# Kernel optimization log

Hardware: AMD Instinct MI355X
Metric: run time of the kernel (lower is better)

## Reference

```python
import jax, jax.numpy as jnp
import numpy as np

N_BISECT_ITERS = 50  # entmax_bisect default


def entmax15_bisect(x):
    """1.5-entmax over the last axis via bisection (alpha=1.5 => p(z)=relu(z)^2)."""
    X = x * 0.5  # multiply by (alpha - 1)
    d = X.shape[-1]
    max_val = jnp.max(X, axis=-1, keepdims=True)
    tau_lo = max_val - 1.0                      # gp(1, alpha) = 1
    tau_hi = max_val - (1.0 / d) ** 0.5         # gp(1/d, alpha)
    f_lo = jnp.sum(jnp.square(jnp.clip(X - tau_lo, 0.0)), -1, keepdims=True) - 1.0

    def body(i, carry):
        tau_lo, dm = carry
        dm = dm * 0.5
        tau_m = tau_lo + dm
        f_m = jnp.sum(jnp.square(jnp.clip(X - tau_m, 0.0)), -1, keepdims=True) - 1.0
        tau_lo = jnp.where(f_m * f_lo >= 0, tau_m, tau_lo)
        return (tau_lo, dm)

    tau_lo, dm = jax.lax.fori_loop(0, N_BISECT_ITERS, body, (tau_lo, tau_hi - tau_lo))
    p = jnp.square(jnp.clip(X - (tau_lo + 0.5 * dm), 0.0))
    return p / jnp.sum(p, axis=-1, keepdims=True)


def entmax_adj(x):
    p = entmax15_bisect(x)
    # straight-through argmax -> one-hot
    k = jnp.argmax(p, axis=-1)
    y_hard = jax.nn.one_hot(k, p.shape[-1], dtype=p.dtype)
    return y_hard - jax.lax.stop_gradient(p) + p


def setup_inputs() -> dict:
    key = jax.random.key(0)
    ks = jax.random.split(key, 7)
    N, D_IN, D_EMB = 524288, 200, 100
    x = jax.random.normal(ks[0], (N, D_IN), dtype=jnp.float32)
    # torch Linear init: U(-1/sqrt(fan_in), 1/sqrt(fan_in))
    def lin(k, out_f, in_f):
        kw, kb = jax.random.split(k)
        bound = 1.0 / np.sqrt(in_f)
        w = jax.random.uniform(kw, (out_f, in_f), jnp.float32, -bound, bound)
        b = jax.random.uniform(kb, (out_f,), jnp.float32, -bound, bound)
        return w, b
    w_out, b_out = lin(ks[1], D_EMB, D_IN)      # fc_out: 200 -> 100
    w_cat, b_cat = lin(ks[2], 2, D_EMB)         # fc_cat: 100 -> 2
    w2, b2 = lin(ks[3], 1, 2)                   # fc2: 2 -> 1
    return {"x": x, "w_out": w_out, "b_out": b_out,
            "w_cat": w_cat, "b_cat": b_cat, "w2": w2, "b2": b2}


def reference(x, w_out, b_out, w_cat, b_cat, w2, b2):
    h = jax.nn.relu(x @ w_out.T + b_out)        # [N, 100]
    logits = h @ w_cat.T + b_cat                # [N, 2]
    adj = entmax_adj(logits)                    # [N, 2] one-hot (straight-through)
    return adj @ w2.T + b2                      # [N, 1]
```

## Files before the change

kernel.cpp:

```cpp
#include <hip/hip_runtime.h>

#define DIN 200
#define DH  100
#define NKT 7
#define MARGIN 2e-3f
#define TR   32
#define NT   8
#define RPB  (NT * TR)

typedef _Float16 half8 __attribute__((ext_vector_type(8)));
typedef _Float16 half4 __attribute__((ext_vector_type(4)));
typedef float f32x4 __attribute__((ext_vector_type(4)));

__device__ inline half8 cvt8(float4 u, float4 v) {
  half8 h;
  h[0] = (_Float16)u.x; h[1] = (_Float16)u.y;
  h[2] = (_Float16)u.z; h[3] = (_Float16)u.w;
  h[4] = (_Float16)v.x; h[5] = (_Float16)v.y;
  h[6] = (_Float16)v.z; h[7] = (_Float16)v.w;
  return h;
}
__device__ inline half4 cvt4(float4 u) {
  half4 h;
  h[0] = (_Float16)u.x; h[1] = (_Float16)u.y;
  h[2] = (_Float16)u.z; h[3] = (_Float16)u.w;
  return h;
}

template <bool HAVE_WS>
__global__ __launch_bounds__(256, 4)
void entmax_sign_mfma(const float* __restrict__ x,
                      const float* __restrict__ w_out,
                      const float* __restrict__ b_out,
                      const float* __restrict__ w_cat,
                      const float* __restrict__ b_cat,
                      const float* __restrict__ w2,
                      const float* __restrict__ b2,
                      float* __restrict__ out,
                      unsigned* __restrict__ cnt,
                      int* __restrict__ list) {
  __shared__ _Float16 axf[14 * 512];
  __shared__ float parts[2][4][TR];

  const int tid  = threadIdx.x;
  const int lane = tid & 63;
  const int wid  = tid >> 6;
  const int arow = lane & 15;
  const int qid  = lane >> 4;

  const float db = b_cat[0] - b_cat[1];
  const float c0 = w2[0] + b2[0];
  const float c1 = w2[1] + b2[0];

  for (int t2 = tid; t2 < 768; t2 += 256) {
    const int fi = t2 / 384, r2 = t2 - fi * 384;
    axf[(fi * 7 + 6) * 512 + 128 + r2] = (_Float16)0.f;
  }

  half8 wf0[NKT], wf1[NKT];
  float bjv0, djv0, bjv1, djv1;
  {
    const int j0 = (2 * wid) * 16 + arow;
    const int j1 = (2 * wid + 1) * 16 + arow;
    bjv0 = (j0 < DH) ? b_out[j0] : 0.f;
    djv0 = (j0 < DH) ? (w_cat[j0] - w_cat[DH + j0]) : 0.f;
    bjv1 = (j1 < DH) ? b_out[j1] : 0.f;
    djv1 = (j1 < DH) ? (w_cat[j1] - w_cat[DH + j1]) : 0.f;
#pragma unroll
    for (int kt = 0; kt < NKT; ++kt) {
      const int k = kt * 32 + qid * 8;
      half8 h0 = {}, h1 = {};
      if (k < DIN) {
        if (j0 < DH) {
          float4 a = *(const float4*)(w_out + j0 * DIN + k);
          float4 b = *(const float4*)(w_out + j0 * DIN + k + 4);
          h0 = cvt8(a, b);
        }
        if (j1 < DH) {
          float4 a = *(const float4*)(w_out + j1 * DIN + k);
          float4 b = *(const float4*)(w_out + j1 * DIN + k + 4);
          h1 = cvt8(a, b);
        }
      }
      wf0[kt] = h0; wf1[kt] = h1;
    }
  }

  const int blockBase = blockIdx.x * RPB;
  const float4* xf4 = (const float4*)x;

  const int row_l = tid & 31;
  const int cseg  = tid >> 5;
  const int wbase = (row_l >> 4) * 7 * 512 + ((row_l & 15) + (cseg >> 1) * 16) * 8
                  + (cseg & 1) * 4;

  float4 u0, u1, u2, u3, u4, u5, u6;
#define LOADT(T)                                                            \
  {                                                                         \
    const float4* xt = xf4 + (size_t)(blockBase + (T) * TR + row_l) * 50 + cseg; \
    u0 = xt[0];  u1 = xt[8];  u2 = xt[16];                                  \
    u3 = xt[24]; u4 = xt[32]; u5 = xt[40];                                  \
    if (cseg < 2) u6 = xt[48];                                              \
  }

  LOADT(0);

#pragma unroll 1
  for (int t = 0; t < NT; ++t) {
    asm volatile("s_waitcnt vmcnt(0)" ::: "memory");
    __builtin_amdgcn_sched_barrier(0);

    *(half4*)(&axf[wbase + 0 * 512]) = cvt4(u0);
    *(half4*)(&axf[wbase + 1 * 512]) = cvt4(u1);
    *(half4*)(&axf[wbase + 2 * 512]) = cvt4(u2);
    *(half4*)(&axf[wbase + 3 * 512]) = cvt4(u3);
    *(half4*)(&axf[wbase + 4 * 512]) = cvt4(u4);
    *(half4*)(&axf[wbase + 5 * 512]) = cvt4(u5);
    if (cseg < 2) *(half4*)(&axf[wbase + 6 * 512]) = cvt4(u6);

    if (t + 1 < NT) LOADT(t + 1);

    asm volatile("s_waitcnt lgkmcnt(0)" ::: "memory");
    __builtin_amdgcn_sched_barrier(0);
    __builtin_amdgcn_s_barrier();

    f32x4 acc[2][2];
#pragma unroll
    for (int rg = 0; rg < 2; ++rg)
#pragma unroll
      for (int jl = 0; jl < 2; ++jl) acc[rg][jl] = (f32x4){0.f, 0.f, 0.f, 0.f};

#pragma unroll
    for (int kt = 0; kt < NKT; ++kt)
#pragma unroll
      for (int rg = 0; rg < 2; ++rg) {
        half8 a = *(half8*)(&axf[(rg * 7 + kt) * 512 + lane * 8]);
        acc[rg][0] = __builtin_amdgcn_mfma_f32_16x16x32_f16(a, wf0[kt], acc[rg][0], 0, 0, 0);
        acc[rg][1] = __builtin_amdgcn_mfma_f32_16x16x32_f16(a, wf1[kt], acc[rg][1], 0, 0, 0);
      }

    f32x4 part[2];
#pragma unroll
    for (int rg = 0; rg < 2; ++rg)
#pragma unroll
      for (int r = 0; r < 4; ++r)
        part[rg][r] = fmaxf(acc[rg][0][r] + bjv0, 0.f) * djv0 +
                      fmaxf(acc[rg][1][r] + bjv1, 0.f) * djv1;
#pragma unroll
    for (int m = 1; m < 16; m <<= 1)
#pragma unroll
      for (int rg = 0; rg < 2; ++rg)
#pragma unroll
        for (int r = 0; r < 4; ++r)
          part[rg][r] += __shfl_xor(part[rg][r], m, 64);

    if (arow == 0) {
      *(f32x4*)(&parts[t & 1][wid][0 * 16 + qid * 4]) = part[0];
      *(f32x4*)(&parts[t & 1][wid][1 * 16 + qid * 4]) = part[1];
    }

    asm volatile("s_waitcnt lgkmcnt(0)" ::: "memory");
    __builtin_amdgcn_sched_barrier(0);
    __builtin_amdgcn_s_barrier();

    if (lane < 8) {
      const int rl = wid * 8 + lane;
      const float delta = parts[t & 1][0][rl] + parts[t & 1][1][rl] +
                          parts[t & 1][2][rl] + parts[t & 1][3][rl] + db;
      const int row = blockBase + t * TR + rl;
      out[row] = (delta >= 0.f) ? c0 : c1;
      if (HAVE_WS) {
        if (fabsf(delta) < MARGIN) {
          const unsigned idx = atomicAdd(cnt, 1u);
          list[idx] = row;
        }
      } else if (fabsf(delta) < MARGIN) {
        const float* xr = x + (size_t)row * DIN;
        double s = (double)b_cat[0] - (double)b_cat[1];
        for (int j = 0; j < DH; ++j) {
          double a = (double)b_out[j];
          for (int k = 0; k < DIN; ++k)
            a += (double)xr[k] * (double)w_out[j * DIN + k];
          if (a > 0.0) s += a * ((double)w_cat[j] - (double)w_cat[DH + j]);
        }
        out[row] = (s >= 0.0) ? c0 : c1;
      }
    }
  }
#undef LOADT
}

__global__ __launch_bounds__(256)
void entmax_fixexact(const float* __restrict__ x,
                     const float* __restrict__ w_out,
                     const float* __restrict__ b_out,
                     const float* __restrict__ w_cat,
                     const float* __restrict__ b_cat,
                     const float* __restrict__ w2,
                     const float* __restrict__ b2,
                     float* __restrict__ out,
                     const unsigned* __restrict__ cnt,
                     const int* __restrict__ list) {
  __shared__ float xs[DIN];
  __shared__ double red[128];
  const int tid = threadIdx.x;
  const unsigned count = *cnt;
  const float c0 = w2[0] + b2[0];
  const float c1 = w2[1] + b2[0];
  const double dbd = (double)b_cat[0] - (double)b_cat[1];

#pragma unroll 1
  for (unsigned i = blockIdx.x; i < count; i += gridDim.x) {
    const int row = list[i];
    if (tid < 50)
      ((float4*)xs)[tid] = ((const float4*)(x + (size_t)row * DIN))[tid];
    __syncthreads();

    double sj = 0.0;
    if (tid < DH) {
      const float4* wr = (const float4*)(w_out + tid * DIN);
      double p0 = 0.0, p1 = 0.0, p2 = 0.0, p3 = 0.0;
#pragma unroll 10
      for (int k4 = 0; k4 < 50; ++k4) {
        const float4 w4 = wr[k4];
        const float4 x4 = ((const float4*)xs)[k4];
        p0 += (double)x4.x * (double)w4.x;
        p1 += (double)x4.y * (double)w4.y;
        p2 += (double)x4.z * (double)w4.z;
        p3 += (double)x4.w * (double)w4.w;
      }
      const double a = ((p0 + p1) + (p2 + p3)) + (double)b_out[tid];
      if (a > 0.0) sj = a * ((double)w_cat[tid] - (double)w_cat[DH + tid]);
    }
    if (tid < 128) red[tid] = (tid < DH) ? sj : 0.0;
    __syncthreads();
    if (tid < 64) {
      double v = red[tid] + red[tid + 64];
#pragma unroll
      for (int s = 1; s < 64; s <<= 1) v += __shfl_xor(v, s, 64);
      if (tid == 0) out[row] = (v + dbd >= 0.0) ? c0 : c1;
    }
    __syncthreads();
  }
}

extern "C" void kernel_launch(void* const* d_in, const int* in_sizes, int n_in,
                              void* d_out, int out_size, void* d_ws, size_t ws_size,
                              hipStream_t stream) {
  const float* x     = (const float*)d_in[0];
  const float* w_out = (const float*)d_in[1];
  const float* b_out = (const float*)d_in[2];
  const float* w_cat = (const float*)d_in[3];
  const float* b_cat = (const float*)d_in[4];
  const float* w2    = (const float*)d_in[5];
  const float* b2    = (const float*)d_in[6];
  float* out = (float*)d_out;

  const int N = in_sizes[0] / DIN;
  const int nblk = N / RPB;

  if (ws_size >= 64 + (size_t)N * sizeof(int)) {
    unsigned* cnt = (unsigned*)d_ws;
    int* list = (int*)((char*)d_ws + 64);
    hipMemsetAsync(d_ws, 0, 64, stream);
    entmax_sign_mfma<true><<<nblk, 256, 0, stream>>>(x, w_out, b_out, w_cat,
                                                     b_cat, w2, b2, out, cnt, list);
    entmax_fixexact<<<512, 256, 0, stream>>>(x, w_out, b_out, w_cat, b_cat,
                                             w2, b2, out, cnt, list);
  } else {
    entmax_sign_mfma<false><<<nblk, 256, 0, stream>>>(x, w_out, b_out, w_cat,
                                                      b_cat, w2, b2, out,
                                                      nullptr, nullptr);
  }
}
```

Before: 130.2 us.

## Double-buffer LDS tiles so staging overlaps MFMA compute

Adds a second LDS buffer for the fp16 x tile. The next tile is now converted and staged into the alternate buffer right after the current tile's MFMAs, and the following global load is issued then. This removes one of the two block barriers per iteration and lets the conversion and LDS writes overlap other waves' compute. It relies on hand-tuned vmcnt counts that allow for the pending output and atomic stores, and it doubles LDS use per block, which could limit occupancy.

Result: no change. 129.3 us (-0.7%).

```diff
diff --git a/kernel.cpp b/kernel.cpp
--- a/kernel.cpp
+++ b/kernel.cpp
@@ -7,6 +7,7 @@
 #define TR   32
 #define NT   8
 #define RPB  (NT * TR)
+#define ABUF (14 * 512)
 
 typedef _Float16 half8 __attribute__((ext_vector_type(8)));
 typedef _Float16 half4 __attribute__((ext_vector_type(4)));
@@ -39,7 +40,7 @@
                       float* __restrict__ out,
                       unsigned* __restrict__ cnt,
                       int* __restrict__ list) {
-  __shared__ _Float16 axf[14 * 512];
+  __shared__ _Float16 axf[2 * ABUF];
   __shared__ float parts[2][4][TR];
 
   const int tid  = threadIdx.x;
@@ -52,9 +53,10 @@
   const float c0 = w2[0] + b2[0];
   const float c1 = w2[1] + b2[0];
 
-  for (int t2 = tid; t2 < 768; t2 += 256) {
-    const int fi = t2 / 384, r2 = t2 - fi * 384;
-    axf[(fi * 7 + 6) * 512 + 128 + r2] = (_Float16)0.f;
+  for (int t2 = tid; t2 < 1536; t2 += 256) {
+    const int b  = t2 / 768, r  = t2 - b * 768;
+    const int fi = r / 384,  r2 = r - fi * 384;
+    axf[b * ABUF + (fi * 7 + 6) * 512 + 128 + r2] = (_Float16)0.f;
   }
 
   half8 wf0[NKT], wf1[NKT];
@@ -102,42 +104,53 @@
     u3 = xt[24]; u4 = xt[32]; u5 = xt[40];                                  \
     if (cseg < 2) u6 = xt[48];                                              \
   }
+#define STAGE(BUF)                                                          \
+  {                                                                         \
+    _Float16* ax = axf + (BUF) * ABUF + wbase;                              \
+    *(half4*)(ax + 0 * 512) = cvt4(u0);                                     \
+    *(half4*)(ax + 1 * 512) = cvt4(u1);                                     \
+    *(half4*)(ax + 2 * 512) = cvt4(u2);                                     \
+    *(half4*)(ax + 3 * 512) = cvt4(u3);                                     \
+    *(half4*)(ax + 4 * 512) = cvt4(u4);                                     \
+    *(half4*)(ax + 5 * 512) = cvt4(u5);                                     \
+    if (cseg < 2) *(half4*)(ax + 6 * 512) = cvt4(u6);                       \
+  }
 
   LOADT(0);
+  asm volatile("s_waitcnt vmcnt(0)" ::: "memory");
+  __builtin_amdgcn_sched_barrier(0);
+  STAGE(0);
+  LOADT(1);
+  asm volatile("s_waitcnt lgkmcnt(0)" ::: "memory");
+  __builtin_amdgcn_sched_barrier(0);
+  __builtin_amdgcn_s_barrier();
 
 #pragma unroll 1
   for (int t = 0; t < NT; ++t) {
-    asm volatile("s_waitcnt vmcnt(0)" ::: "memory");
-    __builtin_amdgcn_sched_barrier(0);
-
-    *(half4*)(&axf[wbase + 0 * 512]) = cvt4(u0);
-    *(half4*)(&axf[wbase + 1 * 512]) = cvt4(u1);
-    *(half4*)(&axf[wbase + 2 * 512]) = cvt4(u2);
-    *(half4*)(&axf[wbase + 3 * 512]) = cvt4(u3);
-    *(half4*)(&axf[wbase + 4 * 512]) = cvt4(u4);
-    *(half4*)(&axf[wbase + 5 * 512]) = cvt4(u5);
-    if (cseg < 2) *(half4*)(&axf[wbase + 6 * 512]) = cvt4(u6);
-
-    if (t + 1 < NT) LOADT(t + 1);
-
-    asm volatile("s_waitcnt lgkmcnt(0)" ::: "memory");
-    __builtin_amdgcn_sched_barrier(0);
-    __builtin_amdgcn_s_barrier();
-
     f32x4 acc[2][2];
 #pragma unroll
     for (int rg = 0; rg < 2; ++rg)
 #pragma unroll
       for (int jl = 0; jl < 2; ++jl) acc[rg][jl] = (f32x4){0.f, 0.f, 0.f, 0.f};
 
+    const _Float16* ab = axf + (t & 1) * ABUF;
 #pragma unroll
     for (int kt = 0; kt < NKT; ++kt)
 #pragma unroll
       for (int rg = 0; rg < 2; ++rg) {
-        half8 a = *(half8*)(&axf[(rg * 7 + kt) * 512 + lane * 8]);
+        half8 a = *(half8*)(ab + (rg * 7 + kt) * 512 + lane * 8);
         acc[rg][0] = __builtin_amdgcn_mfma_f32_16x16x32_f16(a, wf0[kt], acc[rg][0], 0, 0, 0);
         acc[rg][1] = __builtin_amdgcn_mfma_f32_16x16x32_f16(a, wf1[kt], acc[rg][1], 0, 0, 0);
       }
+
+    if (t + 1 < NT) {
+      if (t == 0)      { asm volatile("s_waitcnt vmcnt(0)" ::: "memory"); }
+      else if (HAVE_WS){ asm volatile("s_waitcnt vmcnt(3)" ::: "memory"); }
+      else             { asm volatile("s_waitcnt vmcnt(2)" ::: "memory"); }
+      __builtin_amdgcn_sched_barrier(0);
+      STAGE((t + 1) & 1);
+      if (t + 2 < NT) LOADT(t + 2);
+    }
 
     f32x4 part[2];
 #pragma unroll
@@ -170,6 +183,7 @@
       const int row = blockBase + t * TR + rl;
       out[row] = (delta >= 0.f) ? c0 : c1;
       if (HAVE_WS) {
+        dws_store:
         if (fabsf(delta) < MARGIN) {
           const unsigned idx = atomicAdd(cnt, 1u);
           list[idx] = row;
@@ -188,6 +202,7 @@
     }
   }
 #undef LOADT
+#undef STAGE
 }
 
 __global__ __launch_bounds__(256)
```
